# Performance work log

Hardware: AMD Instinct MI355X
Metric: run time of the kernel (lower is better)

Reference implementation:

```python
import jax
import jax.numpy as jnp
import numpy as np
from jax import lax

DIM = 512
B, T = 8, 2048
DT = 1.0
DT_REF = 1.0
MAX_GROWTH = 0.3


def _xavier(key, shape):
    fan_in, fan_out = shape[1], shape[0]
    lim = float(np.sqrt(6.0 / (fan_in + fan_out)))
    return jax.random.uniform(key, shape, jnp.float32, -lim, lim)


def setup_inputs() -> dict:
    key = jax.random.key(0)
    ks = jax.random.split(key, 10)
    D = DIM
    return {
        "x": jax.random.normal(ks[0], (B, T, D), jnp.float32),
        # ComplexSVDTransform params (U basis is unused by the transform matrix)
        "v_raw_re": jax.random.normal(ks[1], (D, D), jnp.float32) * 0.02,
        "v_raw_im": jax.random.normal(ks[2], (D, D), jnp.float32) * 0.02,
        "log_sigma": jnp.zeros((D,), jnp.float32),
        "dft_weight": jnp.zeros((), jnp.float32),
        # GlobalFluxTracker params (gate_net only used in forward_step; not here)
        "decay_re": jax.random.normal(ks[3], (D,), jnp.float32) * 0.1 - 1.0,
        "decay_im": jax.random.normal(ks[4], (D,), jnp.float32) * 0.1,
        "mix_w": _xavier(ks[5], (2 * D, 2 * D)),
        "mix_b": jnp.zeros((2 * D,), jnp.float32),
        "proj_w": _xavier(ks[6], (2 * D, 2 * D)),
        "proj_b": jnp.zeros((2 * D,), jnp.float32),
        # TemporalPropagator eigenvalue params
        "lam_re": jax.random.normal(ks[7], (D,), jnp.float32) * 0.01,
        "lam_im": jax.random.normal(ks[8], (D,), jnp.float32) * 0.1,
    }


def _cayley(raw_re, raw_im):
    # Q = (I + A_skew)^{-1} (I - A_skew), A_skew = A - A^H
    A = raw_re + 1j * raw_im
    A_skew = A - A.conj().T
    I = jnp.eye(A.shape[0], dtype=A.dtype)
    return jnp.linalg.solve(I + A_skew, I - A_skew)


def _transform_matrix(v_raw_re, v_raw_im, log_sigma, dft_weight):
    V = _cayley(v_raw_re, v_raw_im)
    S = jnp.exp(log_sigma)
    d = v_raw_re.shape[0]
    n = jnp.arange(d, dtype=jnp.float32)
    k = n[:, None]
    dft = jnp.exp(-2j * jnp.pi * (n * k) / d) / jnp.sqrt(jnp.asarray(d, jnp.float32))
    alpha = jax.nn.sigmoid(dft_weight).astype(jnp.complex64)
    V_scaled = V * S[None, :].astype(V.dtype)  # V @ diag(S)
    return V_scaled * (1.0 - alpha) + dft.astype(jnp.complex64) * alpha


def _scan_combine(c1, c2):
    # s_t = a_t * s_{t-1} + b_t  -> associative combine (later element is c2)
    a1, b1 = c1
    a2, b2 = c2
    return (a1 * a2, b1 * a2 + b2)


def reference(x, v_raw_re, v_raw_im, log_sigma, dft_weight,
              decay_re, decay_im, mix_w, mix_b, proj_w, proj_b,
              lam_re, lam_im):
    D = x.shape[-1]
    # --- encode ---
    W = _transform_matrix(v_raw_re, v_raw_im, log_sigma, dft_weight)  # [D,D] complex
    h = jnp.einsum('btd,de->bte', x.astype(jnp.complex64), W)  # [B,T,D] complex
    # --- flux tracker operators ---
    decay = jax.nn.sigmoid(decay_re) + 1j * decay_im  # [D]
    x_cat = jnp.concatenate([h.real, h.imag], axis=-1)  # [B,T,2D]
    x_in = x_cat @ mix_w.T + mix_b
    x_re, x_im = x_in[..., :D], x_in[..., D:]
    X = x_re + 1j * x_im  # forcing [B,T,D]
    A = jnp.broadcast_to(decay.astype(jnp.complex64), h.shape)  # [B,T,D]
    # --- complex diagonal SSM recurrence via parallel scan ---
    _, states = lax.associative_scan(_scan_combine, (A, X.astype(jnp.complex64)), axis=1)
    # --- project states to source ---
    s_cat = jnp.concatenate([states.real, states.imag], axis=-1)
    s_out = s_cat @ proj_w.T + proj_b
    source = s_out[..., :D] + 1j * s_out[..., D:]
    # --- closed-form transition operators ---
    lam = jnp.clip(lam_re, -MAX_GROWTH, MAX_GROWTH) + 1j * lam_im  # [D]
    exp_arg = lam * (DT / DT_REF)
    t_decay = jnp.exp(exp_arg)
    lam_safe = lam + 1e-8 * jnp.sign(lam.real + 1e-12)
    forcing = (jnp.exp(exp_arg) - 1.0) / lam_safe
    h_out = h * t_decay + source * forcing  # [B,T,D]
    # --- decode ---
    W_inv = jnp.linalg.inv(W)
    x_out = jnp.einsum('btd,de->bte', h_out, W_inv)
    return x_out.real


if __name__ == "__main__":
    out = reference(**setup_inputs())
    print(out.shape, out.dtype)
```

## Files before the change

kernel.cpp:

```cpp
#include <hip/hip_runtime.h>
#include <hip/hip_bf16.h>

typedef unsigned short u16;
typedef _Float16 f16x8 __attribute__((ext_vector_type(8)));
typedef float f32x4 __attribute__((ext_vector_type(4)));

#define DEV __device__ __forceinline__

DEV u16 f2h(float f) { _Float16 h = (_Float16)f; u16 u; __builtin_memcpy(&u, &h, 2); return u; }
DEV float h2f(u16 u) { _Float16 h; __builtin_memcpy(&h, &u, 2); return (float)h; }
DEV void splitf(float v, u16& hi, u16& lo) { hi = f2h(v); lo = f2h(v - h2f(hi)); }
DEV float sigm(float x) { return 1.f / (1.f + __expf(-x)); }
DEV void gload16(const u16* g, u16* l) {
  __builtin_amdgcn_global_load_lds((const __attribute__((address_space(1))) void*)g,
                                   (__attribute__((address_space(3))) void*)l, 16, 0, 0);
}

static const int TT = 2048;

static const size_t OFF_AUG    = 0;
static const size_t OFF_WMAT   = OFF_AUG    + (size_t)512*1024*16;
static const size_t OFF_BINV   = OFF_WMAT   + (size_t)512*512*16;
static const size_t OFF_PIV    = OFF_BINV   + (size_t)64*64*16;
static const size_t OFF_TAB    = OFF_PIV    + (size_t)64*1024*16;
static const size_t OFF_WCATH  = OFF_TAB    + (size_t)512*32;
static const size_t OFF_WCATL  = OFF_WCATH  + (size_t)512*1024*2;
static const size_t OFF_MIXH   = OFF_WCATL  + (size_t)512*1024*2;
static const size_t OFF_MIXL   = OFF_MIXH   + (size_t)1024*1024*2;
static const size_t OFF_PROJH  = OFF_MIXL   + (size_t)1024*1024*2;
static const size_t OFF_PROJL  = OFF_PROJH  + (size_t)1024*1024*2;
static const size_t OFF_B1TH   = OFF_PROJL  + (size_t)1024*1024*2;
static const size_t OFF_B1TL   = OFF_B1TH   + (size_t)512*1024*2;
static const size_t OFF_B2TH   = OFF_B1TL   + (size_t)512*1024*2;
static const size_t OFF_B2TL   = OFF_B2TH   + (size_t)512*1024*2;
static const size_t OFF_BTMIXH = OFF_B2TL   + (size_t)512*1024*2;
static const size_t OFF_BTMIXL = OFF_BTMIXH + (size_t)1024*512*2;
static const size_t OFF_BTFH   = OFF_BTMIXL + (size_t)1024*512*2;
static const size_t OFF_BTFL   = OFF_BTFH   + (size_t)512*1536*2;
static const size_t OFF_BIAS2  = OFF_BTFL   + (size_t)512*1536*2;
static const size_t OFF_CARRY  = OFF_BIAS2  + (size_t)512*4;
static const size_t OFF_PREF   = OFF_CARRY  + (size_t)4096*16*8;
static const size_t OFF_XINF   = OFF_PREF   + (size_t)4096*16*8;
static const size_t OFF_ACATH  = OFF_XINF   + (size_t)16384*1024*4;
static const size_t OFF_ACATL  = OFF_ACATH  + (size_t)16384*1536*2;

__global__ __launch_bounds__(256) void k_split_f32(const float* __restrict__ s, u16* __restrict__ dh,
                                                   u16* __restrict__ dl, int n4) {
  int g = blockIdx.x * 256 + threadIdx.x;
  if (g >= n4) return;
  float4 v = ((const float4*)s)[g];
  ushort4 h, l;
  splitf(v.x, h.x, l.x); splitf(v.y, h.y, l.y); splitf(v.z, h.z, l.z); splitf(v.w, h.w, l.w);
  ((ushort4*)dh)[g] = h;
  ((ushort4*)dl)[g] = l;
}

__global__ __launch_bounds__(256) void k_x_to_acat(const float* __restrict__ x, u16* __restrict__ ah,
                                                   u16* __restrict__ al) {
  int g = blockIdx.x * 256 + threadIdx.x;
  if (g >= 2097152) return;
  float4 v = ((const float4*)x)[g];
  int idx = g * 4;
  int row = idx >> 9, col = idx & 511;
  ushort4 h, l;
  splitf(v.x, h.x, l.x); splitf(v.y, h.y, l.y); splitf(v.z, h.z, l.z); splitf(v.w, h.w, l.w);
  *(ushort4*)(ah + (size_t)row*1536 + col) = h;
  *(ushort4*)(al + (size_t)row*1536 + col) = l;
}

__global__ __launch_bounds__(256) void k_transpose_1024(const float* __restrict__ in, u16* __restrict__ oh,
                                                        u16* __restrict__ ol) {
  __shared__ float s[64][65];
  int lx = threadIdx.x & 63, ly = threadIdx.x >> 6;
#pragma unroll
  for (int i = 0; i < 16; ++i) {
    int c = blockIdx.y*64 + ly*16 + i;
    s[ly*16 + i][lx] = in[(size_t)c*1024 + blockIdx.x*64 + lx];
  }
  __syncthreads();
#pragma unroll
  for (int i = 0; i < 16; ++i) {
    int j = blockIdx.x*64 + ly*16 + i;
    u16 h, l; splitf(s[lx][ly*16 + i], h, l);
    oh[(size_t)j*1024 + blockIdx.y*64 + lx] = h;
    ol[(size_t)j*1024 + blockIdx.y*64 + lx] = l;
  }
}

__global__ __launch_bounds__(256) void k_build_aug_f(const float* __restrict__ vre, const float* __restrict__ vim,
                                                     float2* __restrict__ aug) {
  int g = blockIdx.x * 256 + threadIdx.x;
  if (g >= 512*1024) return;
  int i = g >> 10, j = g & 1023;
  int jc = j & 511;
  float sre = vre[i*512 + jc] - vre[jc*512 + i];
  float sim = vim[i*512 + jc] + vim[jc*512 + i];
  float idd = (i == jc) ? 1.f : 0.f;
  aug[g] = (j < 512) ? make_float2(idd + sre, sim) : make_float2(idd - sre, -sim);
}

template<typename T2, typename TR>
__global__ __launch_bounds__(256) void gj_inv64_t(const T2* __restrict__ AUG, T2* __restrict__ BINV, int k0) {
  __shared__ T2 piv[2][68];
  const int tid = threadIdx.x;
  const int r = tid >> 2, q = tid & 3;
  const int lbase = (tid & 63) & ~3;
  T2 a[16];
  const T2* src = AUG + (size_t)(k0 + r)*1024 + k0 + q*16;
#pragma unroll
  for (int jj = 0; jj < 16; ++jj) a[jj] = src[jj];
  for (int pq = 0; pq < 4; ++pq) {
#pragma unroll
    for (int pj = 0; pj < 16; ++pj) {
      const int p = pq*16 + pj;
      const int bu = p & 1;
      if (r == p) {
        TR pvx = __shfl(a[pj].x, lbase + pq, 64);
        TR pvy = __shfl(a[pj].y, lbase + pq, 64);
        TR inv = TR(1) / (pvx*pvx + pvy*pvy);
        T2 pinv; pinv.x = pvx*inv; pinv.y = -pvy*inv;
#pragma unroll
        for (int jj = 0; jj < 16; ++jj) {
          int j = q*16 + jj;
          T2 v;
          if (j == p) v = pinv;
          else { v.x = a[jj].x*pinv.x - a[jj].y*pinv.y; v.y = a[jj].x*pinv.y + a[jj].y*pinv.x; }
          a[jj] = v;
          piv[bu][j + (j >> 4)] = v;
        }
      }
      __syncthreads();
      if (r != p) {
        TR fx = __shfl(a[pj].x, lbase + pq, 64);
        TR fy = __shfl(a[pj].y, lbase + pq, 64);
#pragma unroll
        for (int jj = 0; jj < 16; ++jj) {
          int j = q*16 + jj;
          T2 pv = piv[bu][j + (j >> 4)];
          if (j == p) { a[jj].x = -(fx*pv.x - fy*pv.y); a[jj].y = -(fx*pv.y + fy*pv.x); }
          else        { a[jj].x -=  fx*pv.x - fy*pv.y;  a[jj].y +=  -(fx*pv.y + fy*pv.x); }
        }
      }
    }
  }
  T2* dst = BINV + (size_t)r*64 + q*16;
#pragma unroll
  for (int jj = 0; jj < 16; ++jj) dst[jj] = a[jj];
}

template<typename T2>
__global__ __launch_bounds__(256) void gj_trans_t(const T2* __restrict__ AUG, const T2* __restrict__ BINV,
                                                  T2* __restrict__ PIV, int k0) {
  __shared__ T2 binv[64][16];
  int tid = threadIdx.x;
  int col  = k0 + 64 + blockIdx.x*64 + (tid & 63);
  int rsub = tid >> 6;
  T2 acc[16];
#pragma unroll
  for (int i = 0; i < 16; ++i) { acc[i].x = 0; acc[i].y = 0; }
  for (int kc = 0; kc < 4; ++kc) {
    for (int l = tid; l < 1024; l += 256) {
      int rr = l >> 4, cc = l & 15;
      binv[rr][cc] = BINV[(size_t)rr*64 + kc*16 + cc];
    }
    __syncthreads();
#pragma unroll 4
    for (int kk = 0; kk < 16; ++kk) {
      T2 av = AUG[(size_t)(k0 + kc*16 + kk)*1024 + col];
#pragma unroll
      for (int i = 0; i < 16; ++i) {
        T2 bv = binv[rsub*16 + i][kk];
        acc[i].x += bv.x*av.x - bv.y*av.y;
        acc[i].y += bv.x*av.y + bv.y*av.x;
      }
    }
    __syncthreads();
  }
#pragma unroll
  for (int i = 0; i < 16; ++i) PIV[(size_t)(rsub*16 + i)*1024 + col] = acc[i];
}

template<typename T2>
__global__ __launch_bounds__(256) void gj_update_t(T2* __restrict__ AUG, const T2* __restrict__ PIV, int k0) {
  __shared__ T2 mult[16][64];
  __shared__ T2 pivc[16][64];
  int tid = threadIdx.x;
  int rb = blockIdx.y;
  int colBase = k0 + 64 + blockIdx.x*64;
  for (int l = tid; l < 1024; l += 256) {
    int rr = l >> 6, kk = l & 63;
    mult[rr][kk] = AUG[(size_t)(rb*16 + rr)*1024 + k0 + kk];
  }
  int ccl = tid & 63, rsub = tid >> 6;
  int col = colBase + ccl;
  T2 acc[4];
#pragma unroll
  for (int i = 0; i < 4; ++i) acc[i] = AUG[(size_t)(rb*16 + rsub*4 + i)*1024 + col];
  for (int kc = 0; kc < 4; ++kc) {
    for (int l = tid; l < 1024; l += 256) {
      int rr = l >> 6, cc = l & 63;
      pivc[rr][cc] = PIV[(size_t)(kc*16 + rr)*1024 + colBase + cc];
    }
    __syncthreads();
#pragma unroll 4
    for (int k2 = 0; k2 < 16; ++k2) {
      int kk = kc*16 + k2;
      T2 pv = pivc[k2][ccl];
#pragma unroll
      for (int i = 0; i < 4; ++i) {
        T2 m = mult[rsub*4 + i][kk];
        acc[i].x -= m.x*pv.x - m.y*pv.y;
        acc[i].y -= m.x*pv.y + m.y*pv.x;
      }
    }
    __syncthreads();
  }
#pragma unroll
  for (int i = 0; i < 4; ++i) {
    int gr = rb*16 + rsub*4 + i;
    T2 o = acc[i];
    if (gr >= k0 && gr < k0 + 64) o = PIV[(size_t)(gr - k0)*1024 + col];
    AUG[(size_t)gr*1024 + col] = o;
  }
}

__global__ __launch_bounds__(256) void k_build_w(const float2* __restrict__ aug, const float* __restrict__ lsig,
                                                 const float* __restrict__ dw, double2* __restrict__ wmat,
                                                 u16* __restrict__ wch, u16* __restrict__ wcl) {
  int g = blockIdx.x * 256 + threadIdx.x;
  if (g >= 512*512) return;
  int k = g >> 9, j = g & 511;
  float2 V = aug[(size_t)k*1024 + 512 + j];
  double S = exp((double)lsig[j]);
  double al = 1.0 / (1.0 + exp(-(double)dw[0]));
  double sc = S * (1.0 - al);
  const float n2pi = (float)(-2.0 * 3.14159265358979323846);
  float nk = (float)(k * j);
  float ph32 = (n2pi * nk) / 512.0f;
  double sn, cs; sincos((double)ph32, &sn, &cs);
  float snf = (float)sn, csf = (float)cs;
  float rsq = sqrtf(512.0f);
  float dre = csf / rsq;
  float dimv = snf / rsq;
  double2 w = make_double2((double)V.x*sc + (double)dre*al, (double)V.y*sc + (double)dimv*al);
  wmat[(size_t)k*512 + j] = w;
  u16 h, l;
  splitf((float)w.x, h, l);
  wch[(size_t)k*1024 + j] = h;  wcl[(size_t)k*1024 + j] = l;
  splitf((float)w.y, h, l);
  wch[(size_t)k*1024 + 512 + j] = h;  wcl[(size_t)k*1024 + 512 + j] = l;
}

__global__ __launch_bounds__(256) void k_build_aug2(const double2* __restrict__ wmat, double2* __restrict__ aug) {
  int g = blockIdx.x * 256 + threadIdx.x;
  if (g >= 512*1024) return;
  int i = g >> 10, j = g & 1023;
  aug[g] = (j < 512) ? wmat[(size_t)i*512 + j] : make_double2((j - 512) == i ? 1.0 : 0.0, 0.0);
}

__global__ __launch_bounds__(256) void k_const512(const float* __restrict__ lamre, const float* __restrict__ lamim,
                                                  double4* __restrict__ tab) {
  int g = blockIdx.x * 256 + threadIdx.x;
  if (g >= 512) return;
  double lr = fmin(fmax((double)lamre[g], -0.3), 0.3);
  double li = (double)lamim[g];
  double e = exp(lr);
  double sn, cs; sincos(li, &sn, &cs);
  double tdre = e*cs, tdim = e*sn;
  double sgn = (lr + 1e-12) >= 0.0 ? 1.0 : -1.0;
  double lsr = lr + 1e-8*sgn, lsi = li;
  double numr = tdre - 1.0, numi = tdim;
  double idn = 1.0 / (lsr*lsr + lsi*lsi);
  double fr = (numr*lsr + numi*lsi)*idn;
  double fi = (numi*lsr - numr*lsi)*idn;
  tab[g] = make_double4(tdre, tdim, fr, fi);
}

__global__ __launch_bounds__(256) void k_build_tb(const double2* __restrict__ aug, const double4* __restrict__ tab,
                                                  u16* __restrict__ b1h, u16* __restrict__ b1l,
                                                  u16* __restrict__ b2h, u16* __restrict__ b2l) {
  int g = blockIdx.x * 256 + threadIdx.x;
  if (g >= 512*512) return;
  int e = g & 511, m = g >> 9;
  double2 wv = aug[(size_t)m*1024 + 512 + e];
  double4 tb = tab[m];
  double twre = tb.x*wv.x - tb.y*wv.y, twim = tb.x*wv.y + tb.y*wv.x;
  double fwre = tb.z*wv.x - tb.w*wv.y, fwim = tb.z*wv.y + tb.w*wv.x;
  u16 h, l;
  splitf((float)twre, h, l);  b1h[(size_t)e*1024 + m] = h;        b1l[(size_t)e*1024 + m] = l;
  splitf((float)-twim, h, l); b1h[(size_t)e*1024 + 512 + m] = h;  b1l[(size_t)e*1024 + 512 + m] = l;
  splitf((float)fwre, h, l);  b2h[(size_t)e*1024 + m] = h;        b2l[(size_t)e*1024 + m] = l;
  splitf((float)-fwim, h, l); b2h[(size_t)e*1024 + 512 + m] = h;  b2l[(size_t)e*1024 + 512 + m] = l;
}

__global__ __launch_bounds__(256) void k_bias2(const double2* __restrict__ aug, const double4* __restrict__ tab,
                                               const float* __restrict__ projb, float* __restrict__ bias2) {
  int e = blockIdx.x;
  int t = threadIdx.x;
  double acc = 0.0;
  for (int d = t; d < 512; d += 256) {
    double2 wv = aug[(size_t)d*1024 + 512 + e];
    double4 tb = tab[d];
    double fwre = tb.z*wv.x - tb.w*wv.y;
    double fwim = tb.z*wv.y + tb.w*wv.x;
    acc += (double)projb[d]*fwre - (double)projb[512 + d]*fwim;
  }
#pragma unroll
  for (int off = 32; off; off >>= 1) acc += __shfl_down(acc, off, 64);
  __shared__ double red[4];
  if ((t & 63) == 0) red[t >> 6] = acc;
  __syncthreads();
  if (t == 0) bias2[e] = (float)(red[0] + red[1] + red[2] + red[3]);
}

template<int K, int NOUT, int EPI, int LDA, int LDO>
__global__ __launch_bounds__(256) void gemm3(const u16* __restrict__ Ah, const u16* __restrict__ Al,
                                             const u16* __restrict__ Bh, const u16* __restrict__ Bl,
                                             u16* __restrict__ outH, u16* __restrict__ outL,
                                             float* __restrict__ outF, const float* __restrict__ bias) {
  __shared__ alignas(16) u16 Ash[128*64];
  __shared__ alignas(16) u16 Asl[128*64];
  __shared__ alignas(16) u16 Bsh[128*64];
  __shared__ alignas(16) u16 Bsl[128*64];
  const int tid = threadIdx.x;
  const int lane = tid & 63, wid = tid >> 6;
  const int wr = wid >> 1, wc = wid & 1;
  const int nwg = gridDim.x * gridDim.y;
  const int flatb = blockIdx.y * gridDim.x + blockIdx.x;
  const int chunk = nwg >> 3;
  const int swz = (flatb & 7) * chunk + (flatb >> 3);
  const int rowTile = (swz / gridDim.x) * 128;
  const int colTile = (swz % gridDim.x) * 128;
  f32x4 zz = {0.f, 0.f, 0.f, 0.f};
  f32x4 acc[4][4];
#pragma unroll
  for (int m = 0; m < 4; ++m)
#pragma unroll
    for (int n = 0; n < 4; ++n) acc[m][n] = zz;

  const int KT = K / 64;
  for (int kt = 0; kt < KT; ++kt) {
    const int k0 = kt * 64;
    __syncthreads();
#pragma unroll
    for (int i = 0; i < 4; ++i) {
      int flat = i*256 + tid;
      int ar = flat >> 3;
      int as = (flat & 7) ^ (ar & 7);
      size_t aoff = (size_t)(rowTile + ar)*LDA + (k0 + as*8);
      size_t boff = (size_t)(colTile + ar)*K   + (k0 + as*8);
      int lb = (i*256 + (tid & ~63)) * 8;
      gload16(Ah + aoff, Ash + lb);
      gload16(Al + aoff, Asl + lb);
      gload16(Bh + boff, Bsh + lb);
      gload16(Bl + boff, Bsl + lb);
    }
    __syncthreads();
#pragma unroll
    for (int ks = 0; ks < 2; ++ks) {
      f16x8 afh[4], afl[4], bfh[4], bfl[4];
#pragma unroll
      for (int m = 0; m < 4; ++m) {
        int row = wr*64 + m*16 + (lane & 15);
        int off = row*128 + (((ks*4 + (lane >> 4)) ^ (row & 7)) << 4);
        afh[m] = *(const f16x8*)((const char*)Ash + off);
        afl[m] = *(const f16x8*)((const char*)Asl + off);
      }
#pragma unroll
      for (int n = 0; n < 4; ++n) {
        int row = wc*64 + n*16 + (lane & 15);
        int off = row*128 + (((ks*4 + (lane >> 4)) ^ (row & 7)) << 4);
        bfh[n] = *(const f16x8*)((const char*)Bsh + off);
        bfl[n] = *(const f16x8*)((const char*)Bsl + off);
      }
#pragma unroll
      for (int m = 0; m < 4; ++m)
#pragma unroll
        for (int n = 0; n < 4; ++n) {
          acc[m][n] = __builtin_amdgcn_mfma_f32_16x16x32_f16(afl[m], bfh[n], acc[m][n], 0, 0, 0);
          acc[m][n] = __builtin_amdgcn_mfma_f32_16x16x32_f16(afh[m], bfl[n], acc[m][n], 0, 0, 0);
          acc[m][n] = __builtin_amdgcn_mfma_f32_16x16x32_f16(afh[m], bfh[n], acc[m][n], 0, 0, 0);
        }
    }
  }
  const int colBase = colTile + wc*64;
  const int rowBase = rowTile + wr*64 + (lane >> 4)*4;
#pragma unroll
  for (int n = 0; n < 4; ++n) {
    int col = colBase + n*16 + (lane & 15);
    float bv = (EPI >= 2) ? bias[col] : 0.f;
#pragma unroll
    for (int m = 0; m < 4; ++m) {
#pragma unroll
      for (int j = 0; j < 4; ++j) {
        int row = rowBase + m*16 + j;
        float v = acc[m][n][j] + bv;
        if (EPI >= 2) {
          outF[(size_t)row*LDO + col] = v;
        } else {
          u16 h, l; splitf(v, h, l);
          outH[(size_t)row*LDO + col] = h;
          outL[(size_t)row*LDO + col] = l;
        }
      }
    }
  }
}

__global__ __launch_bounds__(256) void k_scan1(const float* __restrict__ xin, const float* __restrict__ dre_,
                                               const float* __restrict__ dim_, float2* __restrict__ carry) {
  int g = blockIdx.x * 256 + threadIdx.x;
  int d = g & 511; int rr = g >> 9; int b = rr & 7; int c = rr >> 3;
  float dre = sigm(dre_[d]);
  float dim = dim_[d];
  size_t base = ((size_t)(b*TT + c*128))*1024 + d;
  float sre = 0.f, sim = 0.f;
  for (int t = 0; t < 128; ++t) {
    float xre = xin[base];
    float xim = xin[base + 512];
    float nre = dre*sre - dim*sim + xre;
    float nim = dre*sim + dim*sre + xim;
    sre = nre; sim = nim;
    base += 1024;
  }
  carry[((size_t)(b*512 + d))*16 + c] = make_float2(sre, sim);
}

__global__ __launch_bounds__(256) void k_scan2(const float* __restrict__ dre_, const float* __restrict__ dim_,
                                               const float2* __restrict__ carry, float2* __restrict__ pref) {
  int g = blockIdx.x * 256 + threadIdx.x;
  int d = g & 511; int b = g >> 9;
  float dre = sigm(dre_[d]);
  float dim = dim_[d];
  float are = dre, aim = dim;
#pragma unroll
  for (int i = 0; i < 7; ++i) { float nr = are*are - aim*aim; float ni = 2.f*are*aim; are = nr; aim = ni; }
  float sre = 0.f, sim = 0.f;
  size_t base = ((size_t)(b*512 + d))*16;
  for (int c = 0; c < 16; ++c) {
    pref[base + c] = make_float2(sre, sim);
    float2 cr = carry[base + c];
    float nr = are*sre - aim*sim + cr.x;
    float ni = are*sim + aim*sre + cr.y;
    sre = nr; sim = ni;
  }
}

__global__ __launch_bounds__(256) void k_scan3(const float* __restrict__ xin, const float* __restrict__ dre_,
                                               const float* __restrict__ dim_, const float2* __restrict__ pref,
                                               u16* __restrict__ ah, u16* __restrict__ al) {
  int g = blockIdx.x * 256 + threadIdx.x;
  int d = g & 511; int rr = g >> 9; int b = rr & 7; int c = rr >> 3;
  float dre = sigm(dre_[d]);
  float dim = dim_[d];
  float2 p0 = pref[((size_t)(b*512 + d))*16 + c];
  float sre = p0.x, sim = p0.y;
  size_t base  = ((size_t)(b*TT + c*128))*1024 + d;
  size_t base2 = ((size_t)(b*TT + c*128))*1536 + d;
  for (int t = 0; t < 128; ++t) {
    float xre = xin[base];
    float xim = xin[base + 512];
    float nre = dre*sre - dim*sim + xre;
    float nim = dre*sim + dim*sre + xim;
    sre = nre; sim = nim;
    u16 h, l;
    splitf(sre, h, l); ah[base2 + 512]  = h; al[base2 + 512]  = l;
    splitf(sim, h, l); ah[base2 + 1024] = h; al[base2 + 1024] = l;
    base += 1024; base2 += 1536;
  }
}

extern "C" void kernel_launch(void* const* d_in, const int* in_sizes, int n_in,
                              void* d_out, int out_size, void* d_ws, size_t ws_size,
                              hipStream_t stream) {
  (void)in_sizes; (void)n_in; (void)out_size; (void)ws_size;
  const float* x     = (const float*)d_in[0];
  const float* vre   = (const float*)d_in[1];
  const float* vim   = (const float*)d_in[2];
  const float* lsig  = (const float*)d_in[3];
  const float* dw    = (const float*)d_in[4];
  const float* decre = (const float*)d_in[5];
  const float* decim = (const float*)d_in[6];
  const float* mixw  = (const float*)d_in[7];
  const float* mixb  = (const float*)d_in[8];
  const float* projw = (const float*)d_in[9];
  const float* projb = (const float*)d_in[10];
  const float* lamre = (const float*)d_in[11];
  const float* lamim = (const float*)d_in[12];
  float* out = (float*)d_out;
  char* ws = (char*)d_ws;

  double2* AUG    = (double2*)(ws + OFF_AUG);
  float2*  AUGF   = (float2*)(ws + OFF_AUG);
  double2* WMAT   = (double2*)(ws + OFF_WMAT);
  double2* BINV   = (double2*)(ws + OFF_BINV);
  float2*  BINVF  = (float2*)(ws + OFF_BINV);
  double2* PIV    = (double2*)(ws + OFF_PIV);
  float2*  PIVF   = (float2*)(ws + OFF_PIV);
  double4* TAB    = (double4*)(ws + OFF_TAB);
  u16*    WCATH  = (u16*)(ws + OFF_WCATH);
  u16*    WCATL  = (u16*)(ws + OFF_WCATL);
  u16*    MIXH   = (u16*)(ws + OFF_MIXH);
  u16*    MIXL   = (u16*)(ws + OFF_MIXL);
  u16*    PROJH  = (u16*)(ws + OFF_PROJH);
  u16*    PROJL  = (u16*)(ws + OFF_PROJL);
  u16*    B1TH   = (u16*)(ws + OFF_B1TH);
  u16*    B1TL   = (u16*)(ws + OFF_B1TL);
  u16*    B2TH   = (u16*)(ws + OFF_B2TH);
  u16*    B2TL   = (u16*)(ws + OFF_B2TL);
  u16*    BTMIXH = (u16*)(ws + OFF_BTMIXH);
  u16*    BTMIXL = (u16*)(ws + OFF_BTMIXL);
  u16*    BTFH   = (u16*)(ws + OFF_BTFH);
  u16*    BTFL   = (u16*)(ws + OFF_BTFL);
  float*  BIAS2  = (float*)(ws + OFF_BIAS2);
  float2* CARRY  = (float2*)(ws + OFF_CARRY);
  float2* PREF   = (float2*)(ws + OFF_PREF);
  float*  XINF   = (float*)(ws + OFF_XINF);
  u16*    ACATH  = (u16*)(ws + OFF_ACATH);
  u16*    ACATL  = (u16*)(ws + OFF_ACATL);

  k_const512<<<2, 256, 0, stream>>>(lamre, lamim, TAB);
  k_x_to_acat<<<8192, 256, 0, stream>>>(x, ACATH, ACATL);
  k_split_f32<<<1024, 256, 0, stream>>>(mixw, MIXH, MIXL, 262144);
  k_transpose_1024<<<dim3(16, 16), 256, 0, stream>>>(projw, PROJH, PROJL);

  k_build_aug_f<<<2048, 256, 0, stream>>>(vre, vim, AUGF);
  for (int s = 0; s < 8; ++s) {
    int k0 = s * 64;
    int nb = 15 - s;
    gj_inv64_t<float2, float><<<1, 256, 0, stream>>>(AUGF, BINVF, k0);
    gj_trans_t<float2><<<nb, 256, 0, stream>>>(AUGF, BINVF, PIVF, k0);
    gj_update_t<float2><<<dim3(nb, 32), 256, 0, stream>>>(AUGF, PIVF, k0);
  }
  k_build_w<<<1024, 256, 0, stream>>>(AUGF, lsig, dw, WMAT, WCATH, WCATL);

  k_build_aug2<<<2048, 256, 0, stream>>>(WMAT, AUG);
  for (int s = 0; s < 8; ++s) {
    int k0 = s * 64;
    int nb = 15 - s;
    gj_inv64_t<double2, double><<<1, 256, 0, stream>>>(AUG, BINV, k0);
    gj_trans_t<double2><<<nb, 256, 0, stream>>>(AUG, BINV, PIV, k0);
    gj_update_t<double2><<<dim3(nb, 32), 256, 0, stream>>>(AUG, PIV, k0);
  }

  k_build_tb<<<1024, 256, 0, stream>>>(AUG, TAB, B1TH, B1TL, B2TH, B2TL);
  k_bias2<<<512, 256, 0, stream>>>(AUG, TAB, projb, BIAS2);
  gemm3<1024, 512, 0, 1024, 1536><<<dim3(4, 4), 256, 0, stream>>>(B1TH, B1TL, WCATH, WCATL, BTFH, BTFL, nullptr, nullptr);
  gemm3<1024, 1024, 0, 1024, 1536><<<dim3(8, 4), 256, 0, stream>>>(B2TH, B2TL, PROJH, PROJL, BTFH + 512, BTFL + 512, nullptr, nullptr);
  gemm3<1024, 512, 0, 1024, 512><<<dim3(4, 8), 256, 0, stream>>>(MIXH, MIXL, WCATH, WCATL, BTMIXH, BTMIXL, nullptr, nullptr);

  gemm3<512, 1024, 3, 1536, 1024><<<dim3(8, 128), 256, 0, stream>>>(ACATH, ACATL, BTMIXH, BTMIXL, nullptr, nullptr, XINF, mixb);

  k_scan1<<<256, 256, 0, stream>>>(XINF, decre, decim, CARRY);
  k_scan2<<<16, 256, 0, stream>>>(decre, decim, CARRY, PREF);
  k_scan3<<<256, 256, 0, stream>>>(XINF, decre, decim, PREF, ACATH, ACATL);

  gemm3<1536, 512, 2, 1536, 512><<<dim3(4, 128), 256, 0, stream>>>(ACATH, ACATL, BTFH, BTFL, nullptr, nullptr, out, BIAS2);
}
```

Baseline: 2.493 ms.

## Block the 64x64 Gauss-Jordan diagonal inversion into 4x4 panels

```diff
diff --git a/kernel.cpp b/kernel.cpp
--- a/kernel.cpp
+++ b/kernel.cpp
@@ -11,6 +11,9 @@
 DEV float h2f(u16 u) { _Float16 h; __builtin_memcpy(&h, &u, 2); return (float)h; }
 DEV void splitf(float v, u16& hi, u16& lo) { hi = f2h(v); lo = f2h(v - h2f(hi)); }
 DEV float sigm(float x) { return 1.f / (1.f + __expf(-x)); }
+template<typename T2> DEV T2 cml(T2 a, T2 b) { T2 r; r.x = a.x*b.x - a.y*b.y; r.y = a.x*b.y + a.y*b.x; return r; }
+template<typename T2> DEV void cfma_sub(T2& acc, T2 m, T2 p) { acc.x -= m.x*p.x - m.y*p.y; acc.y -= m.x*p.y + m.y*p.x; }
+template<typename T2> DEV void cfma_add(T2& acc, T2 m, T2 p) { acc.x += m.x*p.x - m.y*p.y; acc.y += m.x*p.y + m.y*p.x; }
 DEV void gload16(const u16* g, u16* l) {
   __builtin_amdgcn_global_load_lds((const __attribute__((address_space(1))) void*)g,
                                    (__attribute__((address_space(3))) void*)l, 16, 0, 0);
@@ -100,47 +103,101 @@
 }
 
 template<typename T2, typename TR>
-__global__ __launch_bounds__(256) void gj_inv64_t(const T2* __restrict__ AUG, T2* __restrict__ BINV, int k0) {
-  __shared__ T2 piv[2][68];
+__global__ __launch_bounds__(256) void gj_inv64_b4(const T2* __restrict__ AUG, T2* __restrict__ BINV, int k0) {
+  __shared__ T2 mlt[64][5];
+  __shared__ T2 prow[4][65];
+  __shared__ T2 pscl[4][65];
   const int tid = threadIdx.x;
   const int r = tid >> 2, q = tid & 3;
-  const int lbase = (tid & 63) & ~3;
   T2 a[16];
   const T2* src = AUG + (size_t)(k0 + r)*1024 + k0 + q*16;
 #pragma unroll
   for (int jj = 0; jj < 16; ++jj) a[jj] = src[jj];
-  for (int pq = 0; pq < 4; ++pq) {
-#pragma unroll
-    for (int pj = 0; pj < 16; ++pj) {
-      const int p = pq*16 + pj;
-      const int bu = p & 1;
-      if (r == p) {
-        TR pvx = __shfl(a[pj].x, lbase + pq, 64);
-        TR pvy = __shfl(a[pj].y, lbase + pq, 64);
-        TR inv = TR(1) / (pvx*pvx + pvy*pvy);
-        T2 pinv; pinv.x = pvx*inv; pinv.y = -pvy*inv;
+
+  for (int sq = 0; sq < 4; ++sq) {
+#pragma unroll
+    for (int sj = 0; sj < 4; ++sj) {
+      const int s = sq*4 + sj;
+      const int rb4 = r - 4*s;
+      if (q == sq) {
+#pragma unroll
+        for (int k = 0; k < 4; ++k) mlt[r][k] = a[4*sj + k];
+      }
+      if (rb4 >= 0 && rb4 < 4) {
+#pragma unroll
+        for (int jj = 0; jj < 16; ++jj) prow[rb4][q*16 + jj] = a[jj];
+      }
+      __syncthreads();
+      T2 B[4][4];
+#pragma unroll
+      for (int i2 = 0; i2 < 4; ++i2)
+#pragma unroll
+        for (int j2 = 0; j2 < 4; ++j2) B[i2][j2] = mlt[4*s + i2][j2];
+#pragma unroll
+      for (int p = 0; p < 4; ++p) {
+        T2 pv = B[p][p];
+        TR d = TR(1) / (pv.x*pv.x + pv.y*pv.y);
+        T2 pinv; pinv.x = pv.x*d; pinv.y = -pv.y*d;
+#pragma unroll
+        for (int j2 = 0; j2 < 4; ++j2) B[p][j2] = (j2 == p) ? pinv : cml(B[p][j2], pinv);
+#pragma unroll
+        for (int i2 = 0; i2 < 4; ++i2) {
+          if (i2 == p) continue;
+          T2 f = B[i2][p];
+#pragma unroll
+          for (int j2 = 0; j2 < 4; ++j2) {
+            if (j2 == p) { T2 t = cml(f, pinv); B[i2][j2].x = -t.x; B[i2][j2].y = -t.y; }
+            else cfma_sub(B[i2][j2], f, B[p][j2]);
+          }
+        }
+      }
+      {
+        const int kq = tid >> 6, jc = tid & 63;
+        T2 acc; acc.x = 0; acc.y = 0;
+#pragma unroll
+        for (int kk = 0; kk < 4; ++kk) {
+          if (kq == kk) {
+#pragma unroll
+            for (int t = 0; t < 4; ++t) cfma_add(acc, B[kk][t], prow[t][jc]);
+          }
+        }
+        pscl[kq][jc] = acc;
+      }
+      __syncthreads();
+      if (rb4 >= 0 && rb4 < 4) {
 #pragma unroll
         for (int jj = 0; jj < 16; ++jj) {
-          int j = q*16 + jj;
           T2 v;
-          if (j == p) v = pinv;
-          else { v.x = a[jj].x*pinv.x - a[jj].y*pinv.y; v.y = a[jj].x*pinv.y + a[jj].y*pinv.x; }
+          if ((q == sq) && ((jj >> 2) == sj)) {
+            const int u = jj & 3;
+            v.x = 0; v.y = 0;
+#pragma unroll
+            for (int k = 0; k < 4; ++k) if (rb4 == k) v = B[k][u];
+          } else {
+            v = pscl[rb4][q*16 + jj];
+          }
           a[jj] = v;
-          piv[bu][j + (j >> 4)] = v;
         }
+      } else {
+        T2 m[4];
+#pragma unroll
+        for (int k = 0; k < 4; ++k) m[k] = mlt[r][k];
+#pragma unroll
+        for (int jj = 0; jj < 16; ++jj) {
+          T2 acc = a[jj];
+          if ((q == sq) && ((jj >> 2) == sj)) {
+            const int u = jj & 3;
+            acc.x = 0; acc.y = 0;
+#pragma unroll
+            for (int k = 0; k < 4; ++k) cfma_sub(acc, m[k], B[k][u]);
+          } else {
+#pragma unroll
+            for (int k = 0; k < 4; ++k) cfma_sub(acc, m[k], pscl[k][q*16 + jj]);
+          }
+          a[jj] = acc;
+        }
       }
       __syncthreads();
-      if (r != p) {
-        TR fx = __shfl(a[pj].x, lbase + pq, 64);
-        TR fy = __shfl(a[pj].y, lbase + pq, 64);
-#pragma unroll
-        for (int jj = 0; jj < 16; ++jj) {
-          int j = q*16 + jj;
-          T2 pv = piv[bu][j + (j >> 4)];
-          if (j == p) { a[jj].x = -(fx*pv.x - fy*pv.y); a[jj].y = -(fx*pv.y + fy*pv.x); }
-          else        { a[jj].x -=  fx*pv.x - fy*pv.y;  a[jj].y +=  -(fx*pv.y + fy*pv.x); }
-        }
-      }
     }
   }
   T2* dst = BINV + (size_t)r*64 + q*16;
@@ -528,7 +585,7 @@
   for (int s = 0; s < 8; ++s) {
     int k0 = s * 64;
     int nb = 15 - s;
-    gj_inv64_t<float2, float><<<1, 256, 0, stream>>>(AUGF, BINVF, k0);
+    gj_inv64_b4<float2, float><<<1, 256, 0, stream>>>(AUGF, BINVF, k0);
     gj_trans_t<float2><<<nb, 256, 0, stream>>>(AUGF, BINVF, PIVF, k0);
     gj_update_t<float2><<<dim3(nb, 32), 256, 0, stream>>>(AUGF, PIVF, k0);
   }
@@ -538,7 +595,7 @@
   for (int s = 0; s < 8; ++s) {
     int k0 = s * 64;
     int nb = 15 - s;
-    gj_inv64_t<double2, double><<<1, 256, 0, stream>>>(AUG, BINV, k0);
+    gj_inv64_b4<double2, double><<<1, 256, 0, stream>>>(AUG, BINV, k0);
     gj_trans_t<double2><<<nb, 256, 0, stream>>>(AUG, BINV, PIV, k0);
     gj_update_t<double2><<<dim3(nb, 32), 256, 0, stream>>>(AUG, PIV, k0);
   }
```

After: 2.727 ms. +9.4%, slower.

## Fuse blocked Gauss-Jordan inversion steps into one cooperative kernel with grid syncs

Applied to the files above, without the earlier changes.

```diff
diff --git a/kernel.cpp b/kernel.cpp
--- a/kernel.cpp
+++ b/kernel.cpp
@@ -1,5 +1,8 @@
 #include <hip/hip_runtime.h>
 #include <hip/hip_bf16.h>
+#include <hip/hip_cooperative_groups.h>
+
+namespace cg = cooperative_groups;
 
 typedef unsigned short u16;
 typedef _Float16 f16x8 __attribute__((ext_vector_type(8)));
@@ -100,8 +103,7 @@
 }
 
 template<typename T2, typename TR>
-__global__ __launch_bounds__(256) void gj_inv64_t(const T2* __restrict__ AUG, T2* __restrict__ BINV, int k0) {
-  __shared__ T2 piv[2][68];
+DEV void invA_body(const T2* __restrict__ AUG, T2* __restrict__ BINV, int k0, T2* __restrict__ pivL) {
   const int tid = threadIdx.x;
   const int r = tid >> 2, q = tid & 3;
   const int lbase = (tid & 63) & ~3;
@@ -113,7 +115,7 @@
 #pragma unroll
     for (int pj = 0; pj < 16; ++pj) {
       const int p = pq*16 + pj;
-      const int bu = p & 1;
+      T2* piv = pivL + (p & 1)*68;
       if (r == p) {
         TR pvx = __shfl(a[pj].x, lbase + pq, 64);
         TR pvy = __shfl(a[pj].y, lbase + pq, 64);
@@ -126,7 +128,7 @@
           if (j == p) v = pinv;
           else { v.x = a[jj].x*pinv.x - a[jj].y*pinv.y; v.y = a[jj].x*pinv.y + a[jj].y*pinv.x; }
           a[jj] = v;
-          piv[bu][j + (j >> 4)] = v;
+          piv[j + (j >> 4)] = v;
         }
       }
       __syncthreads();
@@ -136,7 +138,7 @@
 #pragma unroll
         for (int jj = 0; jj < 16; ++jj) {
           int j = q*16 + jj;
-          T2 pv = piv[bu][j + (j >> 4)];
+          T2 pv = piv[j + (j >> 4)];
           if (j == p) { a[jj].x = -(fx*pv.x - fy*pv.y); a[jj].y = -(fx*pv.y + fy*pv.x); }
           else        { a[jj].x -=  fx*pv.x - fy*pv.y;  a[jj].y +=  -(fx*pv.y + fy*pv.x); }
         }
@@ -149,11 +151,10 @@
 }
 
 template<typename T2>
-__global__ __launch_bounds__(256) void gj_trans_t(const T2* __restrict__ AUG, const T2* __restrict__ BINV,
-                                                  T2* __restrict__ PIV, int k0) {
-  __shared__ T2 binv[64][16];
+DEV void transB_body(const T2* __restrict__ AUG, const T2* __restrict__ BINV, T2* __restrict__ PIV,
+                     int k0, int j, T2* __restrict__ binvL ) {
   int tid = threadIdx.x;
-  int col  = k0 + 64 + blockIdx.x*64 + (tid & 63);
+  int col  = k0 + 64 + j*64 + (tid & 63);
   int rsub = tid >> 6;
   T2 acc[16];
 #pragma unroll
@@ -161,7 +162,7 @@
   for (int kc = 0; kc < 4; ++kc) {
     for (int l = tid; l < 1024; l += 256) {
       int rr = l >> 4, cc = l & 15;
-      binv[rr][cc] = BINV[(size_t)rr*64 + kc*16 + cc];
+      binvL[rr*16 + cc] = BINV[(size_t)rr*64 + kc*16 + cc];
     }
     __syncthreads();
 #pragma unroll 4
@@ -169,7 +170,7 @@
       T2 av = AUG[(size_t)(k0 + kc*16 + kk)*1024 + col];
 #pragma unroll
       for (int i = 0; i < 16; ++i) {
-        T2 bv = binv[rsub*16 + i][kk];
+        T2 bv = binvL[(rsub*16 + i)*16 + kk];
         acc[i].x += bv.x*av.x - bv.y*av.y;
         acc[i].y += bv.x*av.y + bv.y*av.x;
       }
@@ -181,15 +182,13 @@
 }
 
 template<typename T2>
-__global__ __launch_bounds__(256) void gj_update_t(T2* __restrict__ AUG, const T2* __restrict__ PIV, int k0) {
-  __shared__ T2 mult[16][64];
-  __shared__ T2 pivc[16][64];
+DEV void updC_body(T2* __restrict__ AUG, const T2* __restrict__ PIV, int k0, int j, int rb,
+                   T2* __restrict__ multL , T2* __restrict__ pivcL ) {
   int tid = threadIdx.x;
-  int rb = blockIdx.y;
-  int colBase = k0 + 64 + blockIdx.x*64;
+  int colBase = k0 + 64 + j*64;
   for (int l = tid; l < 1024; l += 256) {
     int rr = l >> 6, kk = l & 63;
-    mult[rr][kk] = AUG[(size_t)(rb*16 + rr)*1024 + k0 + kk];
+    multL[rr*64 + kk] = AUG[(size_t)(rb*16 + rr)*1024 + k0 + kk];
   }
   int ccl = tid & 63, rsub = tid >> 6;
   int col = colBase + ccl;
@@ -199,16 +198,16 @@
   for (int kc = 0; kc < 4; ++kc) {
     for (int l = tid; l < 1024; l += 256) {
       int rr = l >> 6, cc = l & 63;
-      pivc[rr][cc] = PIV[(size_t)(kc*16 + rr)*1024 + colBase + cc];
+      pivcL[rr*64 + cc] = PIV[(size_t)(kc*16 + rr)*1024 + colBase + cc];
     }
     __syncthreads();
 #pragma unroll 4
     for (int k2 = 0; k2 < 16; ++k2) {
       int kk = kc*16 + k2;
-      T2 pv = pivc[k2][ccl];
+      T2 pv = pivcL[k2*64 + ccl];
 #pragma unroll
       for (int i = 0; i < 4; ++i) {
-        T2 m = mult[rsub*4 + i][kk];
+        T2 m = multL[(rsub*4 + i)*64 + kk];
         acc[i].x -= m.x*pv.x - m.y*pv.y;
         acc[i].y -= m.x*pv.y + m.y*pv.x;
       }
@@ -221,6 +220,32 @@
     T2 o = acc[i];
     if (gr >= k0 && gr < k0 + 64) o = PIV[(size_t)(gr - k0)*1024 + col];
     AUG[(size_t)gr*1024 + col] = o;
+  }
+}
+
+template<typename T2, typename TR>
+__global__ __launch_bounds__(256) void gj_pass(T2* __restrict__ AUG, T2* __restrict__ BINV,
+                                               T2* __restrict__ PIV) {
+  cg::grid_group grid = cg::this_grid();
+  __shared__ __align__(16) char smem[2048 * sizeof(T2)];
+  T2* sm = (T2*)smem;
+  const int bid = blockIdx.x;
+  const int G = gridDim.x;
+  for (int s = 0; s < 8; ++s) {
+    const int k0 = s * 64;
+    const int nb = 15 - s;
+    if (bid == 0) invA_body<T2, TR>(AUG, BINV, k0, sm);
+    __threadfence();
+    grid.sync();
+    for (int j = bid; j < nb; j += G) transB_body<T2>(AUG, BINV, PIV, k0, j, sm);
+    __threadfence();
+    grid.sync();
+    for (int w = bid; w < nb*32; w += G) {
+      int j = w % nb, rb = w / nb;
+      updC_body<T2>(AUG, PIV, k0, j, rb, sm, sm + 1024);
+    }
+    __threadfence();
+    grid.sync();
   }
 }
 
@@ -525,22 +550,18 @@
   k_transpose_1024<<<dim3(16, 16), 256, 0, stream>>>(projw, PROJH, PROJL);
 
   k_build_aug_f<<<2048, 256, 0, stream>>>(vre, vim, AUGF);
-  for (int s = 0; s < 8; ++s) {
-    int k0 = s * 64;
-    int nb = 15 - s;
-    gj_inv64_t<float2, float><<<1, 256, 0, stream>>>(AUGF, BINVF, k0);
-    gj_trans_t<float2><<<nb, 256, 0, stream>>>(AUGF, BINVF, PIVF, k0);
-    gj_update_t<float2><<<dim3(nb, 32), 256, 0, stream>>>(AUGF, PIVF, k0);
+  {
+    float2 *a = AUGF, *b = BINVF, *p = PIVF;
+    void* args[3] = {(void*)&a, (void*)&b, (void*)&p};
+    hipLaunchCooperativeKernel((const void*)gj_pass<float2, float>, dim3(256), dim3(256), args, 0, stream);
   }
   k_build_w<<<1024, 256, 0, stream>>>(AUGF, lsig, dw, WMAT, WCATH, WCATL);
 
   k_build_aug2<<<2048, 256, 0, stream>>>(WMAT, AUG);
-  for (int s = 0; s < 8; ++s) {
-    int k0 = s * 64;
-    int nb = 15 - s;
-    gj_inv64_t<double2, double><<<1, 256, 0, stream>>>(AUG, BINV, k0);
-    gj_trans_t<double2><<<nb, 256, 0, stream>>>(AUG, BINV, PIV, k0);
-    gj_update_t<double2><<<dim3(nb, 32), 256, 0, stream>>>(AUG, PIV, k0);
+  {
+    double2 *a = AUG, *b = BINV, *p = PIV;
+    void* args[3] = {(void*)&a, (void*)&b, (void*)&p};
+    hipLaunchCooperativeKernel((const void*)gj_pass<double2, double>, dim3(256), dim3(256), args, 0, stream);
   }
 
   k_build_tb<<<1024, 256, 0, stream>>>(AUG, TAB, B1TH, B1TL, B2TH, B2TL);
```

Result: slower. 4.250 ms (+70.5%).

## Fuse pivot broadcast into a single-sync step and add spinning warm-up blocks

Applied to the files above, without the earlier changes.

```diff
diff --git a/kernel.cpp b/kernel.cpp
--- a/kernel.cpp
+++ b/kernel.cpp
@@ -43,6 +43,7 @@
 static const size_t OFF_XINF   = OFF_PREF   + (size_t)4096*16*8;
 static const size_t OFF_ACATH  = OFF_XINF   + (size_t)16384*1024*4;
 static const size_t OFF_ACATL  = OFF_ACATH  + (size_t)16384*1536*2;
+static const size_t OFF_FLAGS  = OFF_ACATL  + (size_t)16384*1536*2;
 
 __global__ __launch_bounds__(256) void k_split_f32(const float* __restrict__ s, u16* __restrict__ dh,
                                                    u16* __restrict__ dl, int n4) {
@@ -100,52 +101,90 @@
 }
 
 template<typename T2, typename TR>
-__global__ __launch_bounds__(256) void gj_inv64_t(const T2* __restrict__ AUG, T2* __restrict__ BINV, int k0) {
-  __shared__ T2 piv[2][68];
+DEV void inv64_core(const T2* __restrict__ AUG, T2* __restrict__ BINV, int k0) {
+  __shared__ T2 mcol[2][64];
+  __shared__ T2 praw[2][68];
   const int tid = threadIdx.x;
   const int r = tid >> 2, q = tid & 3;
-  const int lbase = (tid & 63) & ~3;
   T2 a[16];
   const T2* src = AUG + (size_t)(k0 + r)*1024 + k0 + q*16;
 #pragma unroll
   for (int jj = 0; jj < 16; ++jj) a[jj] = src[jj];
+  if (q == 0) mcol[0][r] = a[0];
+  if (r == 0) {
+#pragma unroll
+    for (int jj = 0; jj < 16; ++jj) { int j = q*16 + jj; praw[0][j + (j >> 4)] = a[jj]; }
+  }
+  __syncthreads();
   for (int pq = 0; pq < 4; ++pq) {
 #pragma unroll
     for (int pj = 0; pj < 16; ++pj) {
       const int p = pq*16 + pj;
-      const int bu = p & 1;
+      const int bu = pj & 1;
+      T2 pd = praw[bu][p + (p >> 4)];
+      TR inv = TR(1) / (pd.x*pd.x + pd.y*pd.y);
+      T2 pinv; pinv.x = pd.x*inv; pinv.y = -pd.y*inv;
+      T2 mraw = mcol[bu][r];
+      T2 g; g.x = mraw.x*pinv.x - mraw.y*pinv.y; g.y = mraw.x*pinv.y + mraw.y*pinv.x;
       if (r == p) {
-        TR pvx = __shfl(a[pj].x, lbase + pq, 64);
-        TR pvy = __shfl(a[pj].y, lbase + pq, 64);
-        TR inv = TR(1) / (pvx*pvx + pvy*pvy);
-        T2 pinv; pinv.x = pvx*inv; pinv.y = -pvy*inv;
 #pragma unroll
         for (int jj = 0; jj < 16; ++jj) {
           int j = q*16 + jj;
           T2 v;
           if (j == p) v = pinv;
-          else { v.x = a[jj].x*pinv.x - a[jj].y*pinv.y; v.y = a[jj].x*pinv.y + a[jj].y*pinv.x; }
+          else { T2 pr = praw[bu][j + (j >> 4)]; v.x = pr.x*pinv.x - pr.y*pinv.y; v.y = pr.x*pinv.y + pr.y*pinv.x; }
           a[jj] = v;
-          piv[bu][j + (j >> 4)] = v;
+        }
+      } else {
+#pragma unroll
+        for (int jj = 0; jj < 16; ++jj) {
+          int j = q*16 + jj;
+          if (j == p) { a[jj].x = -g.x; a[jj].y = -g.y; }
+          else {
+            T2 pr = praw[bu][j + (j >> 4)];
+            a[jj].x -= g.x*pr.x - g.y*pr.y;
+            a[jj].y -= g.x*pr.y + g.y*pr.x;
+          }
+        }
+      }
+      if (p < 63) {
+        const int nbu = bu ^ 1;
+        if (q == ((p + 1) >> 4)) mcol[nbu][r] = a[(pj + 1) & 15];
+        if (r == p + 1) {
+#pragma unroll
+          for (int jj = 0; jj < 16; ++jj) { int j = q*16 + jj; praw[nbu][j + (j >> 4)] = a[jj]; }
         }
       }
       __syncthreads();
-      if (r != p) {
-        TR fx = __shfl(a[pj].x, lbase + pq, 64);
-        TR fy = __shfl(a[pj].y, lbase + pq, 64);
-#pragma unroll
-        for (int jj = 0; jj < 16; ++jj) {
-          int j = q*16 + jj;
-          T2 pv = piv[bu][j + (j >> 4)];
-          if (j == p) { a[jj].x = -(fx*pv.x - fy*pv.y); a[jj].y = -(fx*pv.y + fy*pv.x); }
-          else        { a[jj].x -=  fx*pv.x - fy*pv.y;  a[jj].y +=  -(fx*pv.y + fy*pv.x); }
-        }
-      }
     }
   }
   T2* dst = BINV + (size_t)r*64 + q*16;
 #pragma unroll
   for (int jj = 0; jj < 16; ++jj) dst[jj] = a[jj];
+}
+
+template<typename T2, typename TR>
+__global__ __launch_bounds__(256) void gj_inv64_w(const T2* __restrict__ AUG, T2* __restrict__ BINV,
+                                                  int k0, unsigned int* __restrict__ flag) {
+  if (blockIdx.x == 0) {
+    inv64_core<T2, TR>(AUG, BINV, k0);
+    __syncthreads();
+    if (threadIdx.x == 0) { __threadfence(); atomicExch(flag, 1u); }
+  } else {
+    __shared__ int done;
+    if (threadIdx.x == 0) done = 0;
+    __syncthreads();
+    float acc = (float)threadIdx.x + 1.f;
+    for (;;) {
+#pragma unroll
+      for (int i = 0; i < 256; ++i) acc = fmaf(acc, 1.0000001f, 0.5f);
+      if (threadIdx.x == 0) { if (atomicAdd(flag, 0u) != 0u) done = 1; }
+      __syncthreads();
+      if (done) break;
+      __syncthreads();
+    }
+    asm volatile("" :: "v"(acc));
+  }
 }
 
 template<typename T2>
@@ -518,6 +557,9 @@
   float*  XINF   = (float*)(ws + OFF_XINF);
   u16*    ACATH  = (u16*)(ws + OFF_ACATH);
   u16*    ACATL  = (u16*)(ws + OFF_ACATL);
+  unsigned int* FLAGS = (unsigned int*)(ws + OFF_FLAGS);
+
+  hipMemsetAsync(ws + OFF_FLAGS, 0, 256, stream);
 
   k_const512<<<2, 256, 0, stream>>>(lamre, lamim, TAB);
   k_x_to_acat<<<8192, 256, 0, stream>>>(x, ACATH, ACATL);
@@ -528,7 +570,7 @@
   for (int s = 0; s < 8; ++s) {
     int k0 = s * 64;
     int nb = 15 - s;
-    gj_inv64_t<float2, float><<<1, 256, 0, stream>>>(AUGF, BINVF, k0);
+    gj_inv64_w<float2, float><<<256, 256, 0, stream>>>(AUGF, BINVF, k0, FLAGS + s);
     gj_trans_t<float2><<<nb, 256, 0, stream>>>(AUGF, BINVF, PIVF, k0);
     gj_update_t<float2><<<dim3(nb, 32), 256, 0, stream>>>(AUGF, PIVF, k0);
   }
@@ -538,7 +580,7 @@
   for (int s = 0; s < 8; ++s) {
     int k0 = s * 64;
     int nb = 15 - s;
-    gj_inv64_t<double2, double><<<1, 256, 0, stream>>>(AUG, BINV, k0);
+    gj_inv64_w<double2, double><<<256, 256, 0, stream>>>(AUG, BINV, k0, FLAGS + 8 + s);
     gj_trans_t<double2><<<nb, 256, 0, stream>>>(AUG, BINV, PIV, k0);
     gj_update_t<double2><<<dim3(nb, 32), 256, 0, stream>>>(AUG, PIV, k0);
   }
```

Result: slower. 2.647 ms (+6.2%).
